# Performance work log

Hardware: AMD Instinct MI355X
Metric: run time of the kernel (lower is better)

Reference implementation:

```python
import jax, jax.numpy as jnp
import numpy as np

L, B, S, D, F, H = 4, 2, 1024, 1024, 4096, 16
EPS = 1e-5


def setup_inputs() -> dict:
    key = jax.random.key(0)
    ks = jax.random.split(key, 15)
    w = lambda k, shape, s=0.02: (jax.random.normal(k, shape, jnp.float32) * s)
    inp = {
        "x": jax.random.normal(ks[0], (B, S, D), jnp.float32),
        # stacked per-layer params (scanned over leading L axis)
        "ln1_w": jnp.ones((L, D), jnp.float32),
        "ln1_b": jnp.zeros((L, D), jnp.float32),
        "Wq": w(ks[1], (L, D, D)),
        "Wk": w(ks[2], (L, D, D)),
        "Wv": w(ks[3], (L, D, D)),
        "Wo": w(ks[4], (L, D, D)),
        "bo": jnp.zeros((L, D), jnp.float32),
        "ln2_w": jnp.ones((L, D), jnp.float32),
        "ln2_b": jnp.zeros((L, D), jnp.float32),
        "W1": w(ks[5], (L, D, F)),
        "b1": jnp.zeros((L, F), jnp.float32),
        "W2": w(ks[6], (L, F, D)),
        "b2": jnp.zeros((L, D), jnp.float32),
    }
    return inp


def _layernorm(y, w, b):
    m = jnp.mean(y, axis=-1, keepdims=True)
    v = jnp.mean(jnp.square(y - m), axis=-1, keepdims=True)
    return (y - m) * jax.lax.rsqrt(v + EPS) * w + b


def _block(x, p):
    ln1w, ln1b, wq, wk, wv, wo, bo, ln2w, ln2b, w1, b1, w2, b2 = p
    b, s, d = x.shape
    dh = d // H
    scale = dh ** -0.5
    # --- attention sub-block (pre-norm, residual) ---
    h = _layernorm(x, ln1w, ln1b)
    q = (h @ wq).reshape(b, s, H, dh).transpose(0, 2, 1, 3)  # bhsd
    k = (h @ wk).reshape(b, s, H, dh).transpose(0, 2, 1, 3)
    v = (h @ wv).reshape(b, s, H, dh).transpose(0, 2, 1, 3)
    attn = jax.nn.softmax(jnp.einsum("bhqd,bhkd->bhqk", q, k) * scale, axis=-1)
    o = jnp.einsum("bhqk,bhkd->bhqd", attn, v).transpose(0, 2, 1, 3).reshape(b, s, d)
    x = x + (o @ wo + bo)
    # --- FFN sub-block (pre-norm, residual) ---
    h = _layernorm(x, ln2w, ln2b)
    x = x + (jax.nn.gelu(h @ w1 + b1, approximate=False) @ w2 + b2)
    return x, None


def reference(x, ln1_w, ln1_b, Wq, Wk, Wv, Wo, bo, ln2_w, ln2_b, W1, b1, W2, b2):
    xs = (ln1_w, ln1_b, Wq, Wk, Wv, Wo, bo, ln2_w, ln2_b, W1, b1, W2, b2)
    out, _ = jax.lax.scan(_block, x, xs)
    return out
```

## Files before the change

kernel.cpp:

```cpp
#include <hip/hip_runtime.h>
#include <hip/hip_bf16.h>

using bf16   = __bf16;
using bf16x2 = __attribute__((ext_vector_type(2))) __bf16;
using bf16x4 = __attribute__((ext_vector_type(4))) __bf16;
using bf16x8 = __attribute__((ext_vector_type(8))) __bf16;
using f32x4  = __attribute__((ext_vector_type(4))) float;

constexpr int LAYERS = 4;
constexpr int BATCH  = 2;
constexpr int SEQ    = 1024;
constexpr int DIM    = 1024;
constexpr int FF     = 4096;
constexpr int HEADS  = 16;
constexpr int TOK    = BATCH * SEQ;
constexpr int QKVN   = 3 * DIM;
constexpr float EPS  = 1e-5f;

__device__ __forceinline__ void gload_lds16(const void* g, void* l) {
    __builtin_amdgcn_global_load_lds(
        (const __attribute__((address_space(1))) void*)g,
        (__attribute__((address_space(3))) void*)l, 16, 0, 0);
}

__global__ __launch_bounds__(256) void ln_kernel(
    const float* __restrict__ x, const float* __restrict__ g,
    const float* __restrict__ bt, bf16* __restrict__ out)
{
    __shared__ float red[8];
    const int row = blockIdx.x, t = threadIdx.x;
    const float4 v = ((const float4*)(x + (size_t)row * DIM))[t];

    float s = v.x + v.y + v.z + v.w;
    #pragma unroll
    for (int o = 32; o; o >>= 1) s += __shfl_down(s, o, 64);
    if ((t & 63) == 0) red[t >> 6] = s;
    __syncthreads();
    const float mean = (red[0] + red[1] + red[2] + red[3]) * (1.0f / DIM);

    const float dx = v.x - mean, dy = v.y - mean, dz = v.z - mean, dw = v.w - mean;
    float q = dx * dx + dy * dy + dz * dz + dw * dw;
    #pragma unroll
    for (int o = 32; o; o >>= 1) q += __shfl_down(q, o, 64);
    if ((t & 63) == 0) red[4 + (t >> 6)] = q;
    __syncthreads();
    const float var = (red[4] + red[5] + red[6] + red[7]) * (1.0f / DIM);
    const float rstd = rsqrtf(var + EPS);

    const float4 gg = ((const float4*)g)[t];
    const float4 bb = ((const float4*)bt)[t];
    bf16x4 o4;
    o4[0] = (bf16)(dx * rstd * gg.x + bb.x);
    o4[1] = (bf16)(dy * rstd * gg.y + bb.y);
    o4[2] = (bf16)(dz * rstd * gg.z + bb.z);
    o4[3] = (bf16)(dw * rstd * gg.w + bb.w);
    *(bf16x4*)(out + (size_t)row * DIM + t * 4) = o4;
}

template<bool DO_LN>
__global__ __launch_bounds__(256) void lncomb_kernel(
    float* __restrict__ x, const float* __restrict__ p,
    const float* __restrict__ bias, const float* __restrict__ g,
    const float* __restrict__ bt, bf16* __restrict__ out)
{
    __shared__ float red[8];
    const int row = blockIdx.x, t = threadIdx.x;
    float4 v = ((const float4*)(x + (size_t)row * DIM))[t];
    const float4 a0 = ((const float4*)(p + (size_t)row * DIM))[t];
    const float4 a1 = ((const float4*)(p + (size_t)(TOK + row) * DIM))[t];
    const float4 bv = ((const float4*)bias)[t];
    v.x += a0.x + a1.x + bv.x;
    v.y += a0.y + a1.y + bv.y;
    v.z += a0.z + a1.z + bv.z;
    v.w += a0.w + a1.w + bv.w;
    ((float4*)(x + (size_t)row * DIM))[t] = v;
    if (!DO_LN) return;

    float s = v.x + v.y + v.z + v.w;
    #pragma unroll
    for (int o = 32; o; o >>= 1) s += __shfl_down(s, o, 64);
    if ((t & 63) == 0) red[t >> 6] = s;
    __syncthreads();
    const float mean = (red[0] + red[1] + red[2] + red[3]) * (1.0f / DIM);

    const float dx = v.x - mean, dy = v.y - mean, dz = v.z - mean, dw = v.w - mean;
    float q = dx * dx + dy * dy + dz * dz + dw * dw;
    #pragma unroll
    for (int o = 32; o; o >>= 1) q += __shfl_down(q, o, 64);
    if ((t & 63) == 0) red[4 + (t >> 6)] = q;
    __syncthreads();
    const float var = (red[4] + red[5] + red[6] + red[7]) * (1.0f / DIM);
    const float rstd = rsqrtf(var + EPS);

    const float4 gg = ((const float4*)g)[t];
    const float4 bb = ((const float4*)bt)[t];
    bf16x4 o4;
    o4[0] = (bf16)(dx * rstd * gg.x + bb.x);
    o4[1] = (bf16)(dy * rstd * gg.y + bb.y);
    o4[2] = (bf16)(dz * rstd * gg.z + bb.z);
    o4[3] = (bf16)(dw * rstd * gg.w + bb.w);
    *(bf16x4*)(out + (size_t)row * DIM + t * 4) = o4;
}

__global__ __launch_bounds__(256) void wtrans_all_kernel(
    const float* __restrict__ Wq, const float* __restrict__ Wk,
    const float* __restrict__ Wv, const float* __restrict__ Wo,
    const float* __restrict__ W1, const float* __restrict__ W2,
    bf16* __restrict__ wqkvt, bf16* __restrict__ wot,
    bf16* __restrict__ w1t, bf16* __restrict__ w2t)
{
    __shared__ float tile[32][33];
    const int bid = blockIdx.x;
    const float* W; bf16* Wt; int N, K, rowoff, bx, by;
    if (bid < 3072) {
        const int seg = bid >> 10, r = bid & 1023;
        W = (seg == 0) ? Wq : (seg == 1) ? Wk : Wv;
        Wt = wqkvt; N = DIM; K = DIM; rowoff = seg * DIM;
        bx = r & 31; by = r >> 5;
    } else if (bid < 4096) {
        const int r = bid - 3072;
        W = Wo; Wt = wot; N = DIM; K = DIM; rowoff = 0;
        bx = r & 31; by = r >> 5;
    } else if (bid < 8192) {
        const int r = bid - 4096;
        W = W1; Wt = w1t; N = FF; K = DIM; rowoff = 0;
        bx = r & 127; by = r >> 7;
    } else {
        const int r = bid - 8192;
        W = W2; Wt = w2t; N = DIM; K = FF; rowoff = 0;
        bx = r & 31; by = r >> 5;
    }
    const int bn = bx * 32, bk = by * 32;
    const int r = threadIdx.x >> 3, c4 = (threadIdx.x & 7) * 4;
    const float4 v = *(const float4*)(W + (size_t)(bk + r) * N + bn + c4);
    tile[r][c4 + 0] = v.x; tile[r][c4 + 1] = v.y;
    tile[r][c4 + 2] = v.z; tile[r][c4 + 3] = v.w;
    __syncthreads();
    bf16x4 o;
    #pragma unroll
    for (int j = 0; j < 4; ++j) o[j] = (bf16)tile[c4 + j][r];
    *(bf16x4*)(Wt + (size_t)(rowoff + bn + r) * K + bk + c4) = o;
}

template<int BN, int EPI, int SK>
__global__ __launch_bounds__(256) void gemm_kernel(
    const bf16* __restrict__ A, const bf16* __restrict__ Bt,
    const float* __restrict__ bias, void* __restrict__ outv,
    int M, int N, int Kfull)
{
    constexpr int MR  = (BN == 128) ? 4 : 2;
    constexpr int ASZ = 128 * 32, BSZ = BN * 32;
    __shared__ bf16 As[2][ASZ];
    __shared__ bf16 Bs[2][BSZ];

    const int t    = threadIdx.x;
    const int lane = t & 63;
    const int w    = t >> 6;
    const int wm   = (BN == 128) ? (w >> 1) * 64 : w * 32;
    const int wn   = (BN == 128) ? (w & 1) * 64 : 0;
    const int kg   = lane >> 4, lr = lane & 15;

    const int nwg = gridDim.x;
    const int bid = (blockIdx.x & 7) * (nwg >> 3) + (blockIdx.x >> 3);
    const int nbn = N / BN, nbm = M / 128;
    const int ks  = (SK > 1) ? bid / (nbm * nbn) : 0;
    const int r   = (SK > 1) ? bid % (nbm * nbn) : bid;
    const int bm  = ((SK > 1) ? (r / nbn) : (r % nbm)) * 128;
    const int bn  = ((SK > 1) ? (r % nbn) : (r / nbm)) * BN;

    const int Ksl = Kfull / SK;
    const int kof = ks * Ksl;

    f32x4 acc[MR][4] = {};

    auto stage = [&](int buf, int k0) {
        #pragma unroll
        for (int c = 0; c < 2; ++c) {
            const int ci = c * 256 + t;
            gload_lds16(A + (size_t)(bm + (ci >> 2)) * Kfull + kof + k0 + (ci & 3) * 8,
                        &As[buf][ci * 8]);
        }
        #pragma unroll
        for (int c = 0; c < BN / 64; ++c) {
            const int ci = c * 256 + t;
            gload_lds16(Bt + (size_t)(bn + (ci >> 2)) * Kfull + kof + k0 + (ci & 3) * 8,
                        &Bs[buf][ci * 8]);
        }
    };

    stage(0, 0);
    __syncthreads();

    int cur = 0;
    for (int k0 = 0; k0 < Ksl; k0 += 32) {
        if (k0 + 32 < Ksl) stage(cur ^ 1, k0 + 32);

        bf16x8 af[MR], bfr[4];
        #pragma unroll
        for (int m = 0; m < MR; ++m)
            af[m] = *(const bf16x8*)(&As[cur][(wm + m * 16 + lr) * 32 + kg * 8]);
        #pragma unroll
        for (int n = 0; n < 4; ++n)
            bfr[n] = *(const bf16x8*)(&Bs[cur][(wn + n * 16 + lr) * 32 + kg * 8]);
        #pragma unroll
        for (int m = 0; m < MR; ++m)
            #pragma unroll
            for (int n = 0; n < 4; ++n)
                acc[m][n] = __builtin_amdgcn_mfma_f32_16x16x32_bf16(af[m], bfr[n], acc[m][n], 0, 0, 0);

        __syncthreads();
        cur ^= 1;
    }

    #pragma unroll
    for (int m = 0; m < MR; ++m) {
        const int row = bm + wm + m * 16 + kg * 4;
        #pragma unroll
        for (int n = 0; n < 4; ++n) {
            const int col = bn + wn + n * 16 + lr;
            #pragma unroll
            for (int j = 0; j < 4; ++j) {
                const float vv = acc[m][n][j];
                const size_t idx = (size_t)(row + j) * N + col;
                if (EPI == 0) {
                    ((bf16*)outv)[idx] = (bf16)vv;
                } else if (EPI == 1) {
                    const float z = vv + bias[col];
                    const float gl = 0.5f * z * (1.0f + erff(z * 0.70710678118654752f));
                    ((bf16*)outv)[idx] = (bf16)gl;
                } else {
                    ((float*)outv)[(size_t)ks * M * N + idx] = vv;
                }
            }
        }
    }
}

__global__ __launch_bounds__(256) void attn_kernel(
    const bf16* __restrict__ qkv, bf16* __restrict__ od)
{
    __shared__ bf16 Ks[2][64][72];
    __shared__ bf16 Vt[2][64][64];
    __shared__ bf16 Ps[64][72];

    const int nwg = gridDim.x;
    const int bid = (blockIdx.x & 7) * (nwg >> 3) + (blockIdx.x >> 3);
    const int q0  = (bid & 15) * 64;
    const int bh  = bid >> 4;
    const int b   = bh >> 4, h = bh & 15;
    const int t   = threadIdx.x, w = t >> 6, lane = t & 63;
    const int kg  = lane >> 4, lr = lane & 15;

    const bf16* qbase = qkv + (size_t)b * SEQ * QKVN + h * 64;
    const bf16* kbase = qbase + DIM;
    const bf16* vbase = qbase + 2 * DIM;

    bf16x8 qf0, qf1;
    {
        const bf16* qr = qbase + (size_t)(q0 + w * 16 + lr) * QKVN;
        qf0 = *(const bf16x8*)(qr + kg * 8);
        qf1 = *(const bf16x8*)(qr + 32 + kg * 8);
    }

    f32x4 o_acc[4] = {};
    float m_run[4] = {-1e30f, -1e30f, -1e30f, -1e30f};
    float l_run[4] = {};

    const int rK = t >> 3, oK = (t & 7) * 8;
    const int rp = t >> 3, cV = t & 7;

    bf16x8 kr0, kr1, vr0, vr1;
    auto loadKV = [&](int kb) {
        kr0 = *(const bf16x8*)(kbase + (size_t)(kb + rK) * QKVN + oK);
        kr1 = *(const bf16x8*)(kbase + (size_t)(kb + 32 + rK) * QKVN + oK);
        vr0 = *(const bf16x8*)(vbase + (size_t)(kb + 2 * rp) * QKVN + cV * 8);
        vr1 = *(const bf16x8*)(vbase + (size_t)(kb + 2 * rp + 1) * QKVN + cV * 8);
    };
    auto storeKV = [&](int buf) {
        *(bf16x8*)&Ks[buf][rK][oK]      = kr0;
        *(bf16x8*)&Ks[buf][32 + rK][oK] = kr1;
        const int inrow = (((rp >> 2) ^ cV) << 4) | ((rp << 2) & 15);
        #pragma unroll
        for (int j = 0; j < 8; ++j) {
            bf16x2 p; p[0] = vr0[j]; p[1] = vr1[j];
            *(bf16x2*)((char*)&Vt[buf][cV * 8 + j][0] + inrow) = p;
        }
    };

    loadKV(0);
    storeKV(0);
    __syncthreads();

    int cur = 0;
    for (int kb = 0; kb < SEQ; kb += 64) {
        const bool more = (kb + 64 < SEQ);
        if (more) loadKV(kb + 64);

        f32x4 s[4] = {};
        #pragma unroll
        for (int n = 0; n < 4; ++n) {
            const bf16x8 kf0 = *(const bf16x8*)&Ks[cur][n * 16 + lr][kg * 8];
            const bf16x8 kf1 = *(const bf16x8*)&Ks[cur][n * 16 + lr][32 + kg * 8];
            s[n] = __builtin_amdgcn_mfma_f32_16x16x32_bf16(qf0, kf0, s[n], 0, 0, 0);
            s[n] = __builtin_amdgcn_mfma_f32_16x16x32_bf16(qf1, kf1, s[n], 0, 0, 0);
        }
        #pragma unroll
        for (int n = 0; n < 4; ++n) s[n] *= 0.125f;

        float corr[4], rs[4];
        #pragma unroll
        for (int j = 0; j < 4; ++j) {
            float mx = fmaxf(fmaxf(s[0][j], s[1][j]), fmaxf(s[2][j], s[3][j]));
            #pragma unroll
            for (int o = 1; o < 16; o <<= 1) mx = fmaxf(mx, __shfl_xor(mx, o, 64));
            const float mn = fmaxf(m_run[j], mx);
            corr[j] = __expf(m_run[j] - mn);
            m_run[j] = mn;
            rs[j] = 0.f;
        }
        #pragma unroll
        for (int n = 0; n < 4; ++n)
            #pragma unroll
            for (int j = 0; j < 4; ++j) {
                const float e = __expf(s[n][j] - m_run[j]);
                s[n][j] = e; rs[j] += e;
            }
        #pragma unroll
        for (int j = 0; j < 4; ++j) {
            #pragma unroll
            for (int o = 1; o < 16; o <<= 1) rs[j] += __shfl_xor(rs[j], o, 64);
            l_run[j] = l_run[j] * corr[j] + rs[j];
        }
        #pragma unroll
        for (int nd = 0; nd < 4; ++nd)
            #pragma unroll
            for (int j = 0; j < 4; ++j) o_acc[nd][j] *= corr[j];

        #pragma unroll
        for (int n = 0; n < 4; ++n)
            #pragma unroll
            for (int j = 0; j < 4; ++j)
                Ps[w * 16 + kg * 4 + j][n * 16 + lr] = (bf16)s[n][j];

        const bf16x8 pf0 = *(const bf16x8*)&Ps[w * 16 + lr][kg * 8];
        const bf16x8 pf1 = *(const bf16x8*)&Ps[w * 16 + lr][32 + kg * 8];
        #pragma unroll
        for (int nd = 0; nd < 4; ++nd) {
            const int row  = nd * 16 + lr;
            const int crow = (row >> 3) & 7;
            const bf16x8 vf0 = *(const bf16x8*)((const char*)&Vt[cur][row][0] + ((kg ^ crow) << 4));
            const bf16x8 vf1 = *(const bf16x8*)((const char*)&Vt[cur][row][0] + (((4 + kg) ^ crow) << 4));
            o_acc[nd] = __builtin_amdgcn_mfma_f32_16x16x32_bf16(pf0, vf0, o_acc[nd], 0, 0, 0);
            o_acc[nd] = __builtin_amdgcn_mfma_f32_16x16x32_bf16(pf1, vf1, o_acc[nd], 0, 0, 0);
        }

        if (more) storeKV(cur ^ 1);
        __syncthreads();
        cur ^= 1;
    }

    float inv[4];
    #pragma unroll
    for (int j = 0; j < 4; ++j) inv[j] = 1.0f / l_run[j];
    bf16* ob = od + (size_t)(b * SEQ + q0 + w * 16 + kg * 4) * DIM + h * 64;
    #pragma unroll
    for (int nd = 0; nd < 4; ++nd)
        #pragma unroll
        for (int j = 0; j < 4; ++j)
            ob[(size_t)j * DIM + nd * 16 + lr] = (bf16)(o_acc[nd][j] * inv[j]);
}

extern "C" void kernel_launch(void* const* d_in, const int* in_sizes, int n_in,
                              void* d_out, int out_size, void* d_ws, size_t ws_size,
                              hipStream_t stream)
{
    const float* x    = (const float*)d_in[0];
    const float* ln1w = (const float*)d_in[1];
    const float* ln1b = (const float*)d_in[2];
    const float* Wq   = (const float*)d_in[3];
    const float* Wk   = (const float*)d_in[4];
    const float* Wv   = (const float*)d_in[5];
    const float* Wo   = (const float*)d_in[6];
    const float* bo   = (const float*)d_in[7];
    const float* ln2w = (const float*)d_in[8];
    const float* ln2b = (const float*)d_in[9];
    const float* W1   = (const float*)d_in[10];
    const float* b1   = (const float*)d_in[11];
    const float* W2   = (const float*)d_in[12];
    const float* b2   = (const float*)d_in[13];

    char* ws = (char*)d_ws;
    float* xbuf  = (float*)(ws);
    bf16*  hbuf  = (bf16*)(ws + (8ull  << 20));
    bf16*  qkvb  = (bf16*)(ws + (12ull << 20));
    bf16*  obuf  = (bf16*)(ws + (24ull << 20));
    bf16*  gbuf  = (bf16*)(ws + (28ull << 20));
    bf16*  wqkvt = (bf16*)(ws + (44ull << 20));
    bf16*  wot   = (bf16*)(ws + (50ull << 20));
    bf16*  w1t   = (bf16*)(ws + (52ull << 20));
    bf16*  w2t   = (bf16*)(ws + (60ull << 20));
    float* pbuf  = (float*)(ws + (68ull << 20));

    hipMemcpyAsync(xbuf, x, (size_t)TOK * DIM * sizeof(float),
                   hipMemcpyDeviceToDevice, stream);

    const size_t DD = (size_t)DIM * DIM, DF = (size_t)DIM * FF;
    for (int l = 0; l < LAYERS; ++l) {
        wtrans_all_kernel<<<12288, 256, 0, stream>>>(
            Wq + l * DD, Wk + l * DD, Wv + l * DD, Wo + l * DD,
            W1 + l * DF, W2 + l * DF, wqkvt, wot, w1t, w2t);

        if (l == 0)
            ln_kernel<<<TOK, 256, 0, stream>>>(xbuf, ln1w, ln1b, hbuf);

        gemm_kernel<64, 0, 1><<<16 * 48, 256, 0, stream>>>(
            hbuf, wqkvt, nullptr, qkvb, TOK, QKVN, DIM);

        attn_kernel<<<512, 256, 0, stream>>>(qkvb, obuf);

        gemm_kernel<64, 3, 2><<<16 * 8 * 2 * 2, 256, 0, stream>>>(
            obuf, wot, nullptr, pbuf, TOK, DIM, DIM);

        lncomb_kernel<true><<<TOK, 256, 0, stream>>>(
            xbuf, pbuf, bo + l * DIM, ln2w + l * DIM, ln2b + l * DIM, hbuf);

        gemm_kernel<128, 1, 1><<<16 * 32, 256, 0, stream>>>(
            hbuf, w1t, b1 + l * FF, gbuf, TOK, FF, DIM);

        gemm_kernel<64, 3, 2><<<16 * 8 * 2 * 2, 256, 0, stream>>>(
            gbuf, w2t, nullptr, pbuf, TOK, DIM, FF);

        if (l + 1 < LAYERS)
            lncomb_kernel<true><<<TOK, 256, 0, stream>>>(
                xbuf, pbuf, b2 + l * DIM, ln1w + (l + 1) * DIM, ln1b + (l + 1) * DIM, hbuf);
        else
            lncomb_kernel<false><<<TOK, 256, 0, stream>>>(
                xbuf, pbuf, b2 + l * DIM, nullptr, nullptr, nullptr);
    }

    hipMemcpyAsync(d_out, xbuf, (size_t)TOK * DIM * sizeof(float),
                   hipMemcpyDeviceToDevice, stream);
}
```

Measured before the change: 708.5 us.

## Transpose attention MFMAs, pre-scale Q, lazy softmax rescale, vectorized P and output stores

Swaps the MFMA operand order so each lane holds one query row's scores, reducing per-row softmax reductions to two cross-lane shuffles and scalar running max/sum. Folds the 1/8 scale into Q in bf16 once, and only rescales the accumulators when the block max exceeds the running max by more than a threshold (lazy rescaling). P is written per-wave with vector bf16x4 stores, the V transpose swizzle is changed to match, and the output store is vectorized. This cuts VALU/shuffle work in the softmax, at the cost of a small precision change from rounding the scaled Q and the thresholded rescale.

```diff
diff --git a/kernel.cpp b/kernel.cpp
--- a/kernel.cpp
+++ b/kernel.cpp
@@ -241,7 +241,7 @@
 {
     __shared__ bf16 Ks[2][64][72];
     __shared__ bf16 Vt[2][64][64];
-    __shared__ bf16 Ps[64][72];
+    __shared__ bf16 Ps[4][16][72];
 
     const int nwg = gridDim.x;
     const int bid = (blockIdx.x & 7) * (nwg >> 3) + (blockIdx.x >> 3);
@@ -260,11 +260,15 @@
         const bf16* qr = qbase + (size_t)(q0 + w * 16 + lr) * QKVN;
         qf0 = *(const bf16x8*)(qr + kg * 8);
         qf1 = *(const bf16x8*)(qr + 32 + kg * 8);
+        #pragma unroll
+        for (int j = 0; j < 8; ++j) {
+            qf0[j] = (bf16)((float)qf0[j] * 0.125f);
+            qf1[j] = (bf16)((float)qf1[j] * 0.125f);
+        }
     }
 
     f32x4 o_acc[4] = {};
-    float m_run[4] = {-1e30f, -1e30f, -1e30f, -1e30f};
-    float l_run[4] = {};
+    float m_run = -1e30f, l_run = 0.f;
 
     const int rK = t >> 3, oK = (t & 7) * 8;
     const int rp = t >> 3, cV = t & 7;
@@ -279,11 +283,12 @@
     auto storeKV = [&](int buf) {
         *(bf16x8*)&Ks[buf][rK][oK]      = kr0;
         *(bf16x8*)&Ks[buf][32 + rK][oK] = kr1;
-        const int inrow = (((rp >> 2) ^ cV) << 4) | ((rp << 2) & 15);
         #pragma unroll
         for (int j = 0; j < 8; ++j) {
             bf16x2 p; p[0] = vr0[j]; p[1] = vr1[j];
-            *(bf16x2*)((char*)&Vt[buf][cV * 8 + j][0] + inrow) = p;
+            const int d  = cV * 8 + j;
+            const int dw = (((rp >> 2) ^ (j ^ cV)) << 2) | (rp & 3);
+            *(bf16x2*)((char*)&Vt[buf][d][0] + dw * 4) = p;
         }
     };
 
@@ -301,57 +306,59 @@
         for (int n = 0; n < 4; ++n) {
             const bf16x8 kf0 = *(const bf16x8*)&Ks[cur][n * 16 + lr][kg * 8];
             const bf16x8 kf1 = *(const bf16x8*)&Ks[cur][n * 16 + lr][32 + kg * 8];
-            s[n] = __builtin_amdgcn_mfma_f32_16x16x32_bf16(qf0, kf0, s[n], 0, 0, 0);
-            s[n] = __builtin_amdgcn_mfma_f32_16x16x32_bf16(qf1, kf1, s[n], 0, 0, 0);
-        }
-        #pragma unroll
-        for (int n = 0; n < 4; ++n) s[n] *= 0.125f;
-
-        float corr[4], rs[4];
-        #pragma unroll
-        for (int j = 0; j < 4; ++j) {
-            float mx = fmaxf(fmaxf(s[0][j], s[1][j]), fmaxf(s[2][j], s[3][j]));
-            #pragma unroll
-            for (int o = 1; o < 16; o <<= 1) mx = fmaxf(mx, __shfl_xor(mx, o, 64));
-            const float mn = fmaxf(m_run[j], mx);
-            corr[j] = __expf(m_run[j] - mn);
-            m_run[j] = mn;
-            rs[j] = 0.f;
-        }
+            s[n] = __builtin_amdgcn_mfma_f32_16x16x32_bf16(kf0, qf0, s[n], 0, 0, 0);
+            s[n] = __builtin_amdgcn_mfma_f32_16x16x32_bf16(kf1, qf1, s[n], 0, 0, 0);
+        }
+
+        float pmax = -1e30f;
         #pragma unroll
         for (int n = 0; n < 4; ++n)
             #pragma unroll
+            for (int j = 0; j < 4; ++j) pmax = fmaxf(pmax, s[n][j]);
+        pmax = fmaxf(pmax, __shfl_xor(pmax, 16, 64));
+        pmax = fmaxf(pmax, __shfl_xor(pmax, 32, 64));
+
+        if (!__all(pmax <= m_run + 8.0f)) {
+            const float mn   = fmaxf(m_run, pmax);
+            const float corr = __expf(m_run - mn);
+            m_run = mn;
+            l_run *= corr;
+            #pragma unroll
+            for (int nd = 0; nd < 4; ++nd)
+                #pragma unroll
+                for (int j = 0; j < 4; ++j) o_acc[nd][j] *= corr;
+        }
+
+        float rs = 0.f;
+        #pragma unroll
+        for (int n = 0; n < 4; ++n)
+            #pragma unroll
             for (int j = 0; j < 4; ++j) {
-                const float e = __expf(s[n][j] - m_run[j]);
-                s[n][j] = e; rs[j] += e;
+                const float e = __expf(s[n][j] - m_run);
+                s[n][j] = e; rs += e;
             }
-        #pragma unroll
-        for (int j = 0; j < 4; ++j) {
-            #pragma unroll
-            for (int o = 1; o < 16; o <<= 1) rs[j] += __shfl_xor(rs[j], o, 64);
-            l_run[j] = l_run[j] * corr[j] + rs[j];
-        }
-        #pragma unroll
-        for (int nd = 0; nd < 4; ++nd)
-            #pragma unroll
-            for (int j = 0; j < 4; ++j) o_acc[nd][j] *= corr[j];
-
-        #pragma unroll
-        for (int n = 0; n < 4; ++n)
-            #pragma unroll
-            for (int j = 0; j < 4; ++j)
-                Ps[w * 16 + kg * 4 + j][n * 16 + lr] = (bf16)s[n][j];
-
-        const bf16x8 pf0 = *(const bf16x8*)&Ps[w * 16 + lr][kg * 8];
-        const bf16x8 pf1 = *(const bf16x8*)&Ps[w * 16 + lr][32 + kg * 8];
+        rs += __shfl_xor(rs, 16, 64);
+        rs += __shfl_xor(rs, 32, 64);
+        l_run += rs;
+
+        #pragma unroll
+        for (int n = 0; n < 4; ++n) {
+            bf16x4 pw;
+            #pragma unroll
+            for (int j = 0; j < 4; ++j) pw[j] = (bf16)s[n][j];
+            *(bf16x4*)&Ps[w][lr][n * 16 + kg * 4] = pw;
+        }
+
+        const bf16x8 pf0 = *(const bf16x8*)&Ps[w][lr][kg * 8];
+        const bf16x8 pf1 = *(const bf16x8*)&Ps[w][lr][32 + kg * 8];
         #pragma unroll
         for (int nd = 0; nd < 4; ++nd) {
-            const int row  = nd * 16 + lr;
-            const int crow = (row >> 3) & 7;
-            const bf16x8 vf0 = *(const bf16x8*)((const char*)&Vt[cur][row][0] + ((kg ^ crow) << 4));
-            const bf16x8 vf1 = *(const bf16x8*)((const char*)&Vt[cur][row][0] + (((4 + kg) ^ crow) << 4));
-            o_acc[nd] = __builtin_amdgcn_mfma_f32_16x16x32_bf16(pf0, vf0, o_acc[nd], 0, 0, 0);
-            o_acc[nd] = __builtin_amdgcn_mfma_f32_16x16x32_bf16(pf1, vf1, o_acc[nd], 0, 0, 0);
+            const int d   = nd * 16 + lr;
+            const int key = (d ^ (d >> 3)) & 7;
+            const bf16x8 vf0 = *(const bf16x8*)((const char*)&Vt[cur][d][0] + ((kg ^ key) << 4));
+            const bf16x8 vf1 = *(const bf16x8*)((const char*)&Vt[cur][d][0] + (((4 + kg) ^ key) << 4));
+            o_acc[nd] = __builtin_amdgcn_mfma_f32_16x16x32_bf16(vf0, pf0, o_acc[nd], 0, 0, 0);
+            o_acc[nd] = __builtin_amdgcn_mfma_f32_16x16x32_bf16(vf1, pf1, o_acc[nd], 0, 0, 0);
         }
 
         if (more) storeKV(cur ^ 1);
@@ -359,15 +366,15 @@
         cur ^= 1;
     }
 
-    float inv[4];
-    #pragma unroll
-    for (int j = 0; j < 4; ++j) inv[j] = 1.0f / l_run[j];
-    bf16* ob = od + (size_t)(b * SEQ + q0 + w * 16 + kg * 4) * DIM + h * 64;
-    #pragma unroll
-    for (int nd = 0; nd < 4; ++nd)
-        #pragma unroll
-        for (int j = 0; j < 4; ++j)
-            ob[(size_t)j * DIM + nd * 16 + lr] = (bf16)(o_acc[nd][j] * inv[j]);
+    const float inv = 1.0f / l_run;
+    bf16* ob = od + (size_t)(b * SEQ + q0 + w * 16 + lr) * DIM + h * 64;
+    #pragma unroll
+    for (int nd = 0; nd < 4; ++nd) {
+        bf16x4 o4;
+        #pragma unroll
+        for (int j = 0; j < 4; ++j) o4[j] = (bf16)(o_acc[nd][j] * inv);
+        *(bf16x4*)(ob + nd * 16 + kg * 4) = o4;
+    }
 }
 
 extern "C" void kernel_launch(void* const* d_in, const int* in_sizes, int n_in,
```

Result: faster. 650.5 us (-8.2%).
